# Performance work log

Measured on AMD Instinct MI355X. Metric: run time of the kernel, lower is better.

## Reference

```python
import jax, jax.numpy as jnp
import numpy as np

ALPHA = 0.2      # LeakyReLU negative slope
EPS = 1e-5       # LayerNorm eps
NEG = -9e15


def setup_inputs() -> dict:
    key = jax.random.key(0)
    ks = jax.random.split(key, 7)
    B, N, F_in, F_out = 8, 1024, 512, 512
    h1 = jax.random.normal(ks[0], (B, N, F_in), jnp.float32)
    h2 = jax.random.normal(ks[1], (B, N, F_in), jnp.float32)
    adj = jax.random.randint(ks[2], (B, N, N), 0, 2, jnp.int32)
    s = 1.414 * (6.0 / (F_in + F_out)) ** 0.5  # xavier_uniform gain=1.414
    W1 = jax.random.uniform(ks[3], (F_in, F_out), jnp.float32, -s, s)
    W2 = jax.random.uniform(ks[4], (F_in, F_out), jnp.float32, -s, s)
    W3 = jax.random.uniform(ks[5], (F_in, F_out), jnp.float32, -s, s)
    sa = 1.414 * (6.0 / (2 * F_out + 1)) ** 0.5
    a = jax.random.uniform(ks[6], (2 * F_out, 1), jnp.float32, -sa, sa)
    gamma = jnp.ones((F_out,), jnp.float32)
    beta = jnp.zeros((F_out,), jnp.float32)
    return {"h1": h1, "h2": h2, "adj": adj, "W1": W1, "W2": W2,
            "W3": W3, "a": a, "gamma": gamma, "beta": beta}


def reference(h1, h2, adj, W1, W2, W3, a, gamma, beta):
    F_out = W1.shape[1]
    Wh = h1 @ W1                      # [B,N,F]
    Wt = h2 @ W2                      # [B,N,F]
    a1 = a[:F_out, 0]                 # [F]
    a2 = a[F_out:, 0]                 # [F]
    # decomposed edge score: cat([Wh_i, Wt_j]) @ a == Wh_i@a1 + Wt_j@a2
    e = (Wh @ a1)[:, :, None] + (Wt @ a2)[:, None, :]   # [B,N,N]
    e = jnp.where(e > 0, e, ALPHA * e)                  # LeakyReLU
    e = jnp.where(adj > 0, e, NEG)
    attention = jax.nn.softmax(e, axis=2)               # [B,N,N]
    Wv = h2 @ W3                                        # [B,N,F]
    h_prime = attention @ Wv                            # [B,N,F]
    mu = jnp.mean(h_prime, axis=-1, keepdims=True)
    var = jnp.mean(jnp.square(h_prime - mu), axis=-1, keepdims=True)
    h_prime = (h_prime - mu) * jax.lax.rsqrt(var + EPS) * gamma + beta
    return jax.nn.gelu(h_prime, approximate=False)
```

## Files before the change

kernel.cpp:

```cpp
#include <hip/hip_runtime.h>
#include <math.h>

#define ALPHA 0.2f
#define NEGV  -9000000000000000.0f
#define EPSV  1e-5f

static constexpr int Bn = 8;
static constexpr int Nn = 1024;
static constexpr int Fn = 512;
static constexpr int M  = Bn * Nn;

typedef __attribute__((ext_vector_type(8))) short bf16x8;
typedef __attribute__((ext_vector_type(4))) float f32x4;

__device__ inline float wave_reduce_sum(float v) {
#pragma unroll
    for (int off = 32; off; off >>= 1) v += __shfl_xor(v, off);
    return v;
}
__device__ inline float wave_reduce_max(float v) {
#pragma unroll
    for (int off = 32; off; off >>= 1) v = fmaxf(v, __shfl_xor(v, off));
    return v;
}

__device__ inline unsigned short bf16_rne(float f) {
    union { float f; unsigned int u; } v; v.f = f;
    unsigned int r = v.u + 0x7FFFu + ((v.u >> 16) & 1u);
    return (unsigned short)(r >> 16);
}
__device__ inline float bf16_to_f(unsigned short h) {
    union { unsigned int u; float f; } v; v.u = (unsigned int)h << 16;
    return v.f;
}

__global__ __launch_bounds__(256) void k_pack(const int* __restrict__ adj,
                                              unsigned int* __restrict__ pk) {
    int idx = blockIdx.x * 256 + threadIdx.x;
    const int* p = adj + (size_t)idx * 32;
    unsigned int m = 0;
#pragma unroll
    for (int q = 0; q < 8; ++q) {
        int4 v = *(const int4*)&p[q * 4];
        m |= (unsigned)(v.x > 0) << (q * 4 + 0);
        m |= (unsigned)(v.y > 0) << (q * 4 + 1);
        m |= (unsigned)(v.z > 0) << (q * 4 + 2);
        m |= (unsigned)(v.w > 0) << (q * 4 + 3);
    }
    pk[idx] = m;
}

__global__ __launch_bounds__(64) void k_proj_w(const float* __restrict__ W1,
                                               const float* __restrict__ W2,
                                               const float* __restrict__ a,
                                               float* __restrict__ c) {
    int bid = blockIdx.x, which = bid >> 9, row = bid & 511;
    const float* W  = which ? W2 : W1;
    const float* av = a + which * Fn;
    const float* wr = W + (size_t)row * Fn;
    int lane = threadIdx.x;
    float s = 0.f;
#pragma unroll
    for (int p = 0; p < 2; ++p) {
        float4 wv = *(const float4*)&wr[lane * 4 + p * 256];
        float4 a4 = *(const float4*)&av[lane * 4 + p * 256];
        s += wv.x * a4.x + wv.y * a4.y + wv.z * a4.z + wv.w * a4.w;
    }
    s = wave_reduce_sum(s);
    if (lane == 0) c[which * Fn + row] = s;
}

__global__ __launch_bounds__(256) void k_proj_h(const float* __restrict__ h1,
                                                const float* __restrict__ h2,
                                                const float* __restrict__ c,
                                                float* __restrict__ Wha,
                                                float* __restrict__ Wta) {
    int which = blockIdx.y;
    const float* h  = which ? h2 : h1;
    const float* cv = c + which * Fn;
    float* outp = which ? Wta : Wha;
    int wave = threadIdx.x >> 6, lane = threadIdx.x & 63;
    int row  = blockIdx.x * 4 + wave;
    const float* hr = h + (size_t)row * Fn;
    float s = 0.f;
#pragma unroll
    for (int p = 0; p < 2; ++p) {
        float4 hv = *(const float4*)&hr[lane * 8 + p * 4];
        float4 c4 = *(const float4*)&cv[lane * 8 + p * 4];
        s += hv.x * c4.x + hv.y * c4.y + hv.z * c4.z + hv.w * c4.w;
    }
    s = wave_reduce_sum(s);
    if (lane == 0) outp[row] = s;
}

__global__ __launch_bounds__(256) void k_w3t(const float* __restrict__ W3,
                                             unsigned short* __restrict__ hi,
                                             unsigned short* __restrict__ lo) {
    __shared__ float tile[32][33];
    int kt = blockIdx.x * 32, ft = blockIdx.y * 32;
    int c = threadIdx.x & 31, r = threadIdx.x >> 5;
#pragma unroll
    for (int s = 0; s < 4; ++s)
        tile[r + s * 8][c] = W3[(size_t)(kt + r + s * 8) * Fn + ft + c];
    __syncthreads();
#pragma unroll
    for (int s = 0; s < 4; ++s) {
        float f = tile[c][r + s * 8];
        unsigned short h = bf16_rne(f);
        size_t o = (size_t)(ft + r + s * 8) * Fn + kt + c;
        hi[o] = h;
        lo[o] = bf16_rne(f - bf16_to_f(h));
    }
}

__global__ __launch_bounds__(256) void k_gemm2(const float* __restrict__ h2,
                                               const unsigned short* __restrict__ w3h,
                                               const unsigned short* __restrict__ w3l,
                                               unsigned short* __restrict__ wvh,
                                               unsigned short* __restrict__ wvl) {
    __shared__ float etile[64 * 132];
    int t = threadIdx.x, wave = t >> 6, lane = t & 63;
    int l15 = lane & 15, l16 = lane >> 4;
    int i0 = blockIdx.x * 128, f0 = blockIdx.y * 64;
    int wr = wave;

    f32x4 acc[2][4];
#pragma unroll
    for (int mi = 0; mi < 2; ++mi)
#pragma unroll
        for (int nj = 0; nj < 4; ++nj) acc[mi][nj] = (f32x4){0.f, 0.f, 0.f, 0.f};

    const float* a0base = h2 + (size_t)(i0 + wr * 32 + l15) * Fn + l16 * 8;
    const float* a1base = a0base + 16 * Fn;
    const unsigned short* bhb = w3h + (size_t)(f0 + l15) * Fn + l16 * 8;
    const unsigned short* blb = w3l + (size_t)(f0 + l15) * Fn + l16 * 8;

#pragma unroll 2
    for (int kt = 0; kt < Fn / 32; ++kt) {
        bf16x8 bh[4], bl[4];
#pragma unroll
        for (int nj = 0; nj < 4; ++nj) {
            bh[nj] = *(const bf16x8*)(bhb + (size_t)nj * 16 * Fn + kt * 32);
            bl[nj] = *(const bf16x8*)(blb + (size_t)nj * 16 * Fn + kt * 32);
        }
        float4 v0 = *(const float4*)(a0base + kt * 32);
        float4 v1 = *(const float4*)(a0base + kt * 32 + 4);
        float4 v2 = *(const float4*)(a1base + kt * 32);
        float4 v3 = *(const float4*)(a1base + kt * 32 + 4);
        bf16x8 a0, a1;
        {
            const float* f0p = (const float*)&v0;
            const float* f1p = (const float*)&v2;
#pragma unroll
            for (int q = 0; q < 4; ++q) {
                a0[q] = (short)bf16_rne(f0p[q]);
                a1[q] = (short)bf16_rne(f1p[q]);
            }
            const float* g0p = (const float*)&v1;
            const float* g1p = (const float*)&v3;
#pragma unroll
            for (int q = 0; q < 4; ++q) {
                a0[4 + q] = (short)bf16_rne(g0p[q]);
                a1[4 + q] = (short)bf16_rne(g1p[q]);
            }
        }
#pragma unroll
        for (int nj = 0; nj < 4; ++nj) {
            acc[0][nj] = __builtin_amdgcn_mfma_f32_16x16x32_bf16(a0, bh[nj], acc[0][nj], 0, 0, 0);
            acc[0][nj] = __builtin_amdgcn_mfma_f32_16x16x32_bf16(a0, bl[nj], acc[0][nj], 0, 0, 0);
            acc[1][nj] = __builtin_amdgcn_mfma_f32_16x16x32_bf16(a1, bh[nj], acc[1][nj], 0, 0, 0);
            acc[1][nj] = __builtin_amdgcn_mfma_f32_16x16x32_bf16(a1, bl[nj], acc[1][nj], 0, 0, 0);
        }
    }
#pragma unroll
    for (int mi = 0; mi < 2; ++mi)
#pragma unroll
        for (int nj = 0; nj < 4; ++nj) {
            int nloc = wr * 32 + mi * 16 + l16 * 4;
            int floc = nj * 16 + l15;
            *(float4*)&etile[floc * 132 + nloc] = *(float4*)&acc[mi][nj];
        }
    __syncthreads();
    {
        int floc = t >> 2, n0 = (t & 3) * 32;
        int b = i0 >> 10, nb = i0 & 1023;
        unsigned short* oh = wvh + ((size_t)b * Fn + f0 + floc) * Nn + nb + n0;
        unsigned short* ol = wvl + ((size_t)b * Fn + f0 + floc) * Nn + nb + n0;
        const float* src = &etile[floc * 132 + n0];
        bf16x8 rh[4], rl[4];
#pragma unroll
        for (int s = 0; s < 4; ++s) {
#pragma unroll
            for (int q = 0; q < 8; ++q) {
                float f = src[s * 8 + q];
                unsigned short h = bf16_rne(f);
                rh[s][q] = (short)h;
                rl[s][q] = (short)bf16_rne(f - bf16_to_f(h));
            }
        }
#pragma unroll
        for (int s = 0; s < 4; ++s) {
            *(bf16x8*)(oh + s * 8) = rh[s];
            *(bf16x8*)(ol + s * 8) = rl[s];
        }
    }
}

__global__ __launch_bounds__(256) void k_stats(const unsigned int* __restrict__ pk,
                                               const float* __restrict__ Wha,
                                               const float* __restrict__ Wta,
                                               float2* __restrict__ stat) {
    int bi = blockIdx.x;
    int b = bi >> 10;
    const float* wt = Wta + b * Nn;
    float whai = Wha[bi];
    int t = threadIdx.x;
    unsigned int word = pk[(size_t)bi * 32 + (t >> 3)];
    int sh = (t & 7) * 4;
    float4 wv = *(const float4*)&wt[t * 4];
    float e[4];
    {
        float x;
        x = whai + wv.x; x = fmaxf(x, ALPHA * x); e[0] = ((word >> (sh + 0)) & 1) ? x : NEGV;
        x = whai + wv.y; x = fmaxf(x, ALPHA * x); e[1] = ((word >> (sh + 1)) & 1) ? x : NEGV;
        x = whai + wv.z; x = fmaxf(x, ALPHA * x); e[2] = ((word >> (sh + 2)) & 1) ? x : NEGV;
        x = whai + wv.w; x = fmaxf(x, ALPHA * x); e[3] = ((word >> (sh + 3)) & 1) ? x : NEGV;
    }
    float m4 = fmaxf(fmaxf(e[0], e[1]), fmaxf(e[2], e[3]));
    __shared__ float redm[4], reds[4];
    int wave = t >> 6, lane = t & 63;
    float m = wave_reduce_max(m4);
    if (lane == 0) redm[wave] = m;
    __syncthreads();
    m = fmaxf(fmaxf(redm[0], redm[1]), fmaxf(redm[2], redm[3]));
    float s4 = __expf(e[0] - m) + __expf(e[1] - m) + __expf(e[2] - m) + __expf(e[3] - m);
    float s = wave_reduce_sum(s4);
    if (lane == 0) reds[wave] = s;
    __syncthreads();
    if (t == 0) {
        s = reds[0] + reds[1] + reds[2] + reds[3];
        stat[bi] = make_float2(m, 1.0f / s);
    }
}

__global__ __launch_bounds__(256) void k_attn2(const unsigned int* __restrict__ pk,
                                               const float* __restrict__ Wha,
                                               const float* __restrict__ Wta,
                                               const float2* __restrict__ stat,
                                               const unsigned short* __restrict__ wvh,
                                               const unsigned short* __restrict__ wvl,
                                               float* __restrict__ outp) {
    __shared__ unsigned int pkt[32 * 128];
    __shared__ float wta_s[Nn];
    __shared__ float wha_s[128], m_s[128], rs_s[128];
    int t = threadIdx.x, wave = t >> 6, lane = t & 63;
    int l15 = lane & 15, l16 = lane >> 4;
    int f0 = blockIdx.x * 64, i0 = blockIdx.y * 128, b = blockIdx.z;

    {
        int r = t >> 1, half = t & 1;
        const unsigned int* src = pk + ((size_t)(b * Nn + i0 + r)) * 32 + half * 16;
        uint4 w0 = *(const uint4*)src, w1 = *(const uint4*)(src + 4);
        uint4 w2 = *(const uint4*)(src + 8), w3 = *(const uint4*)(src + 12);
        const unsigned int* ww = (const unsigned int*)&w0;
        unsigned int wv_[16] = {w0.x, w0.y, w0.z, w0.w, w1.x, w1.y, w1.z, w1.w,
                                w2.x, w2.y, w2.z, w2.w, w3.x, w3.y, w3.z, w3.w};
        (void)ww;
#pragma unroll
        for (int w = 0; w < 16; ++w) pkt[(half * 16 + w) * 128 + r] = wv_[w];
        *(float4*)&wta_s[t * 4] = *(const float4*)&Wta[b * Nn + t * 4];
        if (t < 128) {
            wha_s[t] = Wha[b * Nn + i0 + t];
            float2 st = stat[b * Nn + i0 + t];
            m_s[t] = st.x; rs_s[t] = st.y;
        }
    }
    __syncthreads();

    int wr = wave;
    float whaA = wha_s[wr * 32 + l15],      mA = m_s[wr * 32 + l15];
    float whaB = wha_s[wr * 32 + 16 + l15], mB = m_s[wr * 32 + 16 + l15];
    const unsigned short* bhb = wvh + ((size_t)b * Fn + f0 + l15) * Nn + l16 * 8;
    const unsigned short* blb = wvl + ((size_t)b * Fn + f0 + l15) * Nn + l16 * 8;

    f32x4 acc[2][4];
#pragma unroll
    for (int mi = 0; mi < 2; ++mi)
#pragma unroll
        for (int nj = 0; nj < 4; ++nj) acc[mi][nj] = (f32x4){0.f, 0.f, 0.f, 0.f};

#pragma unroll 2
    for (int kt = 0; kt < Nn / 32; ++kt) {
        bf16x8 bh[4], bl[4];
#pragma unroll
        for (int nj = 0; nj < 4; ++nj) {
            bh[nj] = *(const bf16x8*)(bhb + (size_t)nj * 16 * Nn + kt * 32);
            bl[nj] = *(const bf16x8*)(blb + (size_t)nj * 16 * Nn + kt * 32);
        }
        unsigned int shA = pkt[kt * 128 + wr * 32 + l15] >> (l16 * 8);
        unsigned int shB = pkt[kt * 128 + wr * 32 + 16 + l15] >> (l16 * 8);
        float4 wq0 = *(const float4*)&wta_s[kt * 32 + l16 * 8];
        float4 wq1 = *(const float4*)&wta_s[kt * 32 + l16 * 8 + 4];
        float wq[8] = {wq0.x, wq0.y, wq0.z, wq0.w, wq1.x, wq1.y, wq1.z, wq1.w};
        bf16x8 a0, a1;
#pragma unroll
        for (int q = 0; q < 8; ++q) {
            float xA = whaA + wq[q];
            xA = fmaxf(xA, ALPHA * xA);
            float pA = __expf(xA - mA);
            pA = ((shA >> q) & 1) ? pA : 0.0f;
            a0[q] = (short)bf16_rne(pA);
            float xB = whaB + wq[q];
            xB = fmaxf(xB, ALPHA * xB);
            float pB = __expf(xB - mB);
            pB = ((shB >> q) & 1) ? pB : 0.0f;
            a1[q] = (short)bf16_rne(pB);
        }
#pragma unroll
        for (int nj = 0; nj < 4; ++nj) {
            acc[0][nj] = __builtin_amdgcn_mfma_f32_16x16x32_bf16(a0, bh[nj], acc[0][nj], 0, 0, 0);
            acc[0][nj] = __builtin_amdgcn_mfma_f32_16x16x32_bf16(a0, bl[nj], acc[0][nj], 0, 0, 0);
            acc[1][nj] = __builtin_amdgcn_mfma_f32_16x16x32_bf16(a1, bh[nj], acc[1][nj], 0, 0, 0);
            acc[1][nj] = __builtin_amdgcn_mfma_f32_16x16x32_bf16(a1, bl[nj], acc[1][nj], 0, 0, 0);
        }
    }
#pragma unroll
    for (int mi = 0; mi < 2; ++mi)
#pragma unroll
        for (int nj = 0; nj < 4; ++nj) {
#pragma unroll
            for (int r = 0; r < 4; ++r) {
                int rloc = wr * 32 + mi * 16 + l16 * 4 + r;
                float rs = rs_s[rloc];
                outp[((size_t)b * Nn + i0 + rloc) * Fn + f0 + nj * 16 + l15] =
                    rs * acc[mi][nj][r];
            }
        }
}

__global__ __launch_bounds__(128) void k_ln_gelu(float* __restrict__ x,
                                                 const float* __restrict__ gamma,
                                                 const float* __restrict__ beta) {
    int row = blockIdx.x;
    float* xr = x + (size_t)row * Fn;
    int t = threadIdx.x;
    float4 v = *(float4*)&xr[t * 4];
    float s = v.x + v.y + v.z + v.w;
    float q = v.x * v.x + v.y * v.y + v.z * v.z + v.w * v.w;
    s = wave_reduce_sum(s);
    q = wave_reduce_sum(q);
    __shared__ float rs[2], rq[2];
    int wave = t >> 6, lane = t & 63;
    if (lane == 0) { rs[wave] = s; rq[wave] = q; }
    __syncthreads();
    s = rs[0] + rs[1];
    q = rq[0] + rq[1];
    float mu   = s * (1.0f / Fn);
    float var  = q * (1.0f / Fn) - mu * mu;
    float rstd = rsqrtf(var + EPSV);
    float4 g  = *(const float4*)&gamma[t * 4];
    float4 be = *(const float4*)&beta[t * 4];
    auto gel = [](float xx) { return 0.5f * xx * (1.0f + erff(xx * 0.70710678118f)); };
    float y0 = (v.x - mu) * rstd * g.x + be.x;
    float y1 = (v.y - mu) * rstd * g.y + be.y;
    float y2 = (v.z - mu) * rstd * g.z + be.z;
    float y3 = (v.w - mu) * rstd * g.w + be.w;
    float4 o = {gel(y0), gel(y1), gel(y2), gel(y3)};
    *(float4*)&xr[t * 4] = o;
}

extern "C" void kernel_launch(void* const* d_in, const int* in_sizes, int n_in,
                              void* d_out, int out_size, void* d_ws, size_t ws_size,
                              hipStream_t stream) {
    const float* h1    = (const float*)d_in[0];
    const float* h2    = (const float*)d_in[1];
    const int*   adj   = (const int*)d_in[2];
    const float* W1    = (const float*)d_in[3];
    const float* W2    = (const float*)d_in[4];
    const float* W3    = (const float*)d_in[5];
    const float* a     = (const float*)d_in[6];
    const float* gamma = (const float*)d_in[7];
    const float* beta  = (const float*)d_in[8];
    float* outp = (float*)d_out;

    unsigned short* wvh  = (unsigned short*)d_ws;
    unsigned short* wvl  = wvh + (size_t)M * Fn;
    unsigned short* w3h  = wvl + (size_t)M * Fn;
    unsigned short* w3l  = w3h + (size_t)Fn * Fn;
    unsigned int*   pack = (unsigned int*)(w3l + (size_t)Fn * Fn);
    float2*         stat = (float2*)(pack + (size_t)M * 32);
    float*          c    = (float*)(stat + M);
    float*          Wha  = c + 1024;
    float*          Wta  = Wha + M;

    hipLaunchKernelGGL(k_pack, dim3(M * 32 / 256), dim3(256), 0, stream, adj, pack);
    hipLaunchKernelGGL(k_proj_w, dim3(1024), dim3(64), 0, stream, W1, W2, a, c);
    hipLaunchKernelGGL(k_proj_h, dim3(M / 4, 2), dim3(256), 0, stream, h1, h2, c, Wha, Wta);
    hipLaunchKernelGGL(k_w3t, dim3(16, 16), dim3(256), 0, stream, W3, w3h, w3l);
    hipLaunchKernelGGL(k_gemm2, dim3(M / 128, Fn / 64), dim3(256), 0, stream,
                       h2, w3h, w3l, wvh, wvl);
    hipLaunchKernelGGL(k_stats, dim3(M), dim3(256), 0, stream, pack, Wha, Wta, stat);
    hipLaunchKernelGGL(k_attn2, dim3(Fn / 64, Nn / 128, Bn), dim3(256), 0, stream,
                       pack, Wha, Wta, stat, wvh, wvl, outp);
    hipLaunchKernelGGL(k_ln_gelu, dim3(M), dim3(128), 0, stream, outp, gamma, beta);
}
```

Measured before the change: 245.5 us.

## Fuse adjacency packing with softmax stats and halve GEMM row tiles

Merges the adjacency bit-packing kernel and the row softmax-statistics kernel into one pass over adj, so the packed mask is not written and then reread by a separate launch. The value GEMM and the attention GEMM now use 64-row tiles with one 16-row MFMA strip per wave and launch_bounds hinting four blocks per CU. This doubles the grid and lowers register pressure to raise occupancy, at the cost of less reuse of each B-fragment load across rows. The hand-written bf16 rounding is also replaced with the HIP intrinsic.

```diff
diff --git a/kernel.cpp b/kernel.cpp
--- a/kernel.cpp
+++ b/kernel.cpp
@@ -1,4 +1,5 @@
 #include <hip/hip_runtime.h>
+#include <hip/hip_bf16.h>
 #include <math.h>
 
 #define ALPHA 0.2f
@@ -24,30 +25,13 @@
     return v;
 }
 
-__device__ inline unsigned short bf16_rne(float f) {
-    union { float f; unsigned int u; } v; v.f = f;
-    unsigned int r = v.u + 0x7FFFu + ((v.u >> 16) & 1u);
-    return (unsigned short)(r >> 16);
-}
-__device__ inline float bf16_to_f(unsigned short h) {
-    union { unsigned int u; float f; } v; v.u = (unsigned int)h << 16;
+__device__ inline short f2bf(float f) {
+    __hip_bfloat16 h = __float2bfloat16(f);
+    return *reinterpret_cast<short*>(&h);
+}
+__device__ inline float bf2f(short s) {
+    union { unsigned int u; float f; } v; v.u = (unsigned int)(unsigned short)s << 16;
     return v.f;
-}
-
-__global__ __launch_bounds__(256) void k_pack(const int* __restrict__ adj,
-                                              unsigned int* __restrict__ pk) {
-    int idx = blockIdx.x * 256 + threadIdx.x;
-    const int* p = adj + (size_t)idx * 32;
-    unsigned int m = 0;
-#pragma unroll
-    for (int q = 0; q < 8; ++q) {
-        int4 v = *(const int4*)&p[q * 4];
-        m |= (unsigned)(v.x > 0) << (q * 4 + 0);
-        m |= (unsigned)(v.y > 0) << (q * 4 + 1);
-        m |= (unsigned)(v.z > 0) << (q * 4 + 2);
-        m |= (unsigned)(v.w > 0) << (q * 4 + 3);
-    }
-    pk[idx] = m;
 }
 
 __global__ __launch_bounds__(64) void k_proj_w(const float* __restrict__ W1,
@@ -93,6 +77,54 @@
     if (lane == 0) outp[row] = s;
 }
 
+__global__ __launch_bounds__(256) void k_packstats(const int* __restrict__ adj,
+                                                   const float* __restrict__ Wha,
+                                                   const float* __restrict__ Wta,
+                                                   unsigned int* __restrict__ pk,
+                                                   float2* __restrict__ stat) {
+    int bi = blockIdx.x;
+    int b = bi >> 10;
+    const int*   arow = adj + (size_t)bi * Nn;
+    const float* wt   = Wta + b * Nn;
+    float whai = Wha[bi];
+    int t = threadIdx.x;
+    int4   av = *(const int4*)&arow[t * 4];
+    float4 wv = *(const float4*)&wt[t * 4];
+    unsigned int nib = (unsigned)(av.x > 0) | ((unsigned)(av.y > 0) << 1) |
+                       ((unsigned)(av.z > 0) << 2) | ((unsigned)(av.w > 0) << 3);
+    float e[4];
+    {
+        float x;
+        x = whai + wv.x; x = fmaxf(x, ALPHA * x); e[0] = (nib & 1) ? x : NEGV;
+        x = whai + wv.y; x = fmaxf(x, ALPHA * x); e[1] = (nib & 2) ? x : NEGV;
+        x = whai + wv.z; x = fmaxf(x, ALPHA * x); e[2] = (nib & 4) ? x : NEGV;
+        x = whai + wv.w; x = fmaxf(x, ALPHA * x); e[3] = (nib & 8) ? x : NEGV;
+    }
+    __shared__ unsigned char nibs[256];
+    __shared__ float redm[4], reds[4];
+    nibs[t] = (unsigned char)nib;
+    int wave = t >> 6, lane = t & 63;
+    float m4 = fmaxf(fmaxf(e[0], e[1]), fmaxf(e[2], e[3]));
+    float m = wave_reduce_max(m4);
+    if (lane == 0) redm[wave] = m;
+    __syncthreads();
+    m = fmaxf(fmaxf(redm[0], redm[1]), fmaxf(redm[2], redm[3]));
+    float s4 = __expf(e[0] - m) + __expf(e[1] - m) + __expf(e[2] - m) + __expf(e[3] - m);
+    float s = wave_reduce_sum(s4);
+    if (lane == 0) reds[wave] = s;
+    __syncthreads();
+    if (t < 32) {
+        unsigned int w = 0;
+#pragma unroll
+        for (int u = 0; u < 8; ++u) w |= ((unsigned int)nibs[t * 8 + u]) << (4 * u);
+        pk[(size_t)bi * 32 + t] = w;
+    }
+    if (t == 0) {
+        s = reds[0] + reds[1] + reds[2] + reds[3];
+        stat[bi] = make_float2(m, 1.0f / s);
+    }
+}
+
 __global__ __launch_bounds__(256) void k_w3t(const float* __restrict__ W3,
                                              unsigned short* __restrict__ hi,
                                              unsigned short* __restrict__ lo) {
@@ -106,32 +138,28 @@
 #pragma unroll
     for (int s = 0; s < 4; ++s) {
         float f = tile[c][r + s * 8];
-        unsigned short h = bf16_rne(f);
+        short h = f2bf(f);
         size_t o = (size_t)(ft + r + s * 8) * Fn + kt + c;
-        hi[o] = h;
-        lo[o] = bf16_rne(f - bf16_to_f(h));
-    }
-}
-
-__global__ __launch_bounds__(256) void k_gemm2(const float* __restrict__ h2,
-                                               const unsigned short* __restrict__ w3h,
-                                               const unsigned short* __restrict__ w3l,
-                                               unsigned short* __restrict__ wvh,
-                                               unsigned short* __restrict__ wvl) {
-    __shared__ float etile[64 * 132];
+        hi[o] = (unsigned short)h;
+        lo[o] = (unsigned short)f2bf(f - bf2f(h));
+    }
+}
+
+__global__ __launch_bounds__(256, 4) void k_gemm3(const float* __restrict__ h2,
+                                                  const unsigned short* __restrict__ w3h,
+                                                  const unsigned short* __restrict__ w3l,
+                                                  unsigned short* __restrict__ wvh,
+                                                  unsigned short* __restrict__ wvl) {
+    __shared__ float etile[64 * 68];
     int t = threadIdx.x, wave = t >> 6, lane = t & 63;
     int l15 = lane & 15, l16 = lane >> 4;
-    int i0 = blockIdx.x * 128, f0 = blockIdx.y * 64;
-    int wr = wave;
-
-    f32x4 acc[2][4];
-#pragma unroll
-    for (int mi = 0; mi < 2; ++mi)
-#pragma unroll
-        for (int nj = 0; nj < 4; ++nj) acc[mi][nj] = (f32x4){0.f, 0.f, 0.f, 0.f};
-
-    const float* a0base = h2 + (size_t)(i0 + wr * 32 + l15) * Fn + l16 * 8;
-    const float* a1base = a0base + 16 * Fn;
+    int i0 = blockIdx.x * 64, f0 = blockIdx.y * 64;
+
+    f32x4 acc[4];
+#pragma unroll
+    for (int nj = 0; nj < 4; ++nj) acc[nj] = (f32x4){0.f, 0.f, 0.f, 0.f};
+
+    const float* abase = h2 + (size_t)(i0 + wave * 16 + l15) * Fn + l16 * 8;
     const unsigned short* bhb = w3h + (size_t)(f0 + l15) * Fn + l16 * 8;
     const unsigned short* blb = w3l + (size_t)(f0 + l15) * Fn + l16 * 8;
 
@@ -143,133 +171,68 @@
             bh[nj] = *(const bf16x8*)(bhb + (size_t)nj * 16 * Fn + kt * 32);
             bl[nj] = *(const bf16x8*)(blb + (size_t)nj * 16 * Fn + kt * 32);
         }
-        float4 v0 = *(const float4*)(a0base + kt * 32);
-        float4 v1 = *(const float4*)(a0base + kt * 32 + 4);
-        float4 v2 = *(const float4*)(a1base + kt * 32);
-        float4 v3 = *(const float4*)(a1base + kt * 32 + 4);
-        bf16x8 a0, a1;
-        {
-            const float* f0p = (const float*)&v0;
-            const float* f1p = (const float*)&v2;
-#pragma unroll
-            for (int q = 0; q < 4; ++q) {
-                a0[q] = (short)bf16_rne(f0p[q]);
-                a1[q] = (short)bf16_rne(f1p[q]);
-            }
-            const float* g0p = (const float*)&v1;
-            const float* g1p = (const float*)&v3;
-#pragma unroll
-            for (int q = 0; q < 4; ++q) {
-                a0[4 + q] = (short)bf16_rne(g0p[q]);
-                a1[4 + q] = (short)bf16_rne(g1p[q]);
-            }
-        }
+        float4 v0 = *(const float4*)(abase + kt * 32);
+        float4 v1 = *(const float4*)(abase + kt * 32 + 4);
+        bf16x8 a0;
+        a0[0] = f2bf(v0.x); a0[1] = f2bf(v0.y); a0[2] = f2bf(v0.z); a0[3] = f2bf(v0.w);
+        a0[4] = f2bf(v1.x); a0[5] = f2bf(v1.y); a0[6] = f2bf(v1.z); a0[7] = f2bf(v1.w);
 #pragma unroll
         for (int nj = 0; nj < 4; ++nj) {
-            acc[0][nj] = __builtin_amdgcn_mfma_f32_16x16x32_bf16(a0, bh[nj], acc[0][nj], 0, 0, 0);
-            acc[0][nj] = __builtin_amdgcn_mfma_f32_16x16x32_bf16(a0, bl[nj], acc[0][nj], 0, 0, 0);
-            acc[1][nj] = __builtin_amdgcn_mfma_f32_16x16x32_bf16(a1, bh[nj], acc[1][nj], 0, 0, 0);
-            acc[1][nj] = __builtin_amdgcn_mfma_f32_16x16x32_bf16(a1, bl[nj], acc[1][nj], 0, 0, 0);
-        }
-    }
-#pragma unroll
-    for (int mi = 0; mi < 2; ++mi)
-#pragma unroll
-        for (int nj = 0; nj < 4; ++nj) {
-            int nloc = wr * 32 + mi * 16 + l16 * 4;
-            int floc = nj * 16 + l15;
-            *(float4*)&etile[floc * 132 + nloc] = *(float4*)&acc[mi][nj];
-        }
+            acc[nj] = __builtin_amdgcn_mfma_f32_16x16x32_bf16(a0, bh[nj], acc[nj], 0, 0, 0);
+            acc[nj] = __builtin_amdgcn_mfma_f32_16x16x32_bf16(a0, bl[nj], acc[nj], 0, 0, 0);
+        }
+    }
+#pragma unroll
+    for (int nj = 0; nj < 4; ++nj) {
+        int floc = nj * 16 + l15;
+        int nloc = wave * 16 + l16 * 4;
+        *(f32x4*)&etile[floc * 68 + nloc] = acc[nj];
+    }
     __syncthreads();
     {
-        int floc = t >> 2, n0 = (t & 3) * 32;
-        int b = i0 >> 10, nb = i0 & 1023;
-        unsigned short* oh = wvh + ((size_t)b * Fn + f0 + floc) * Nn + nb + n0;
-        unsigned short* ol = wvl + ((size_t)b * Fn + f0 + floc) * Nn + nb + n0;
-        const float* src = &etile[floc * 132 + n0];
-        bf16x8 rh[4], rl[4];
-#pragma unroll
-        for (int s = 0; s < 4; ++s) {
-#pragma unroll
-            for (int q = 0; q < 8; ++q) {
-                float f = src[s * 8 + q];
-                unsigned short h = bf16_rne(f);
-                rh[s][q] = (short)h;
-                rl[s][q] = (short)bf16_rne(f - bf16_to_f(h));
-            }
-        }
-#pragma unroll
-        for (int s = 0; s < 4; ++s) {
-            *(bf16x8*)(oh + s * 8) = rh[s];
-            *(bf16x8*)(ol + s * 8) = rl[s];
-        }
-    }
-}
-
-__global__ __launch_bounds__(256) void k_stats(const unsigned int* __restrict__ pk,
-                                               const float* __restrict__ Wha,
-                                               const float* __restrict__ Wta,
-                                               float2* __restrict__ stat) {
-    int bi = blockIdx.x;
-    int b = bi >> 10;
-    const float* wt = Wta + b * Nn;
-    float whai = Wha[bi];
-    int t = threadIdx.x;
-    unsigned int word = pk[(size_t)bi * 32 + (t >> 3)];
-    int sh = (t & 7) * 4;
-    float4 wv = *(const float4*)&wt[t * 4];
-    float e[4];
-    {
-        float x;
-        x = whai + wv.x; x = fmaxf(x, ALPHA * x); e[0] = ((word >> (sh + 0)) & 1) ? x : NEGV;
-        x = whai + wv.y; x = fmaxf(x, ALPHA * x); e[1] = ((word >> (sh + 1)) & 1) ? x : NEGV;
-        x = whai + wv.z; x = fmaxf(x, ALPHA * x); e[2] = ((word >> (sh + 2)) & 1) ? x : NEGV;
-        x = whai + wv.w; x = fmaxf(x, ALPHA * x); e[3] = ((word >> (sh + 3)) & 1) ? x : NEGV;
-    }
-    float m4 = fmaxf(fmaxf(e[0], e[1]), fmaxf(e[2], e[3]));
-    __shared__ float redm[4], reds[4];
-    int wave = t >> 6, lane = t & 63;
-    float m = wave_reduce_max(m4);
-    if (lane == 0) redm[wave] = m;
-    __syncthreads();
-    m = fmaxf(fmaxf(redm[0], redm[1]), fmaxf(redm[2], redm[3]));
-    float s4 = __expf(e[0] - m) + __expf(e[1] - m) + __expf(e[2] - m) + __expf(e[3] - m);
-    float s = wave_reduce_sum(s4);
-    if (lane == 0) reds[wave] = s;
-    __syncthreads();
-    if (t == 0) {
-        s = reds[0] + reds[1] + reds[2] + reds[3];
-        stat[bi] = make_float2(m, 1.0f / s);
-    }
-}
-
-__global__ __launch_bounds__(256) void k_attn2(const unsigned int* __restrict__ pk,
-                                               const float* __restrict__ Wha,
-                                               const float* __restrict__ Wta,
-                                               const float2* __restrict__ stat,
-                                               const unsigned short* __restrict__ wvh,
-                                               const unsigned short* __restrict__ wvl,
-                                               float* __restrict__ outp) {
-    __shared__ unsigned int pkt[32 * 128];
+        int floc = t >> 2, ic = (t & 3) * 16;
+        int b = i0 >> 10, nb = (i0 & 1023) + ic;
+        const float* src = &etile[floc * 68 + ic];
+        unsigned short* oh = wvh + ((size_t)b * Fn + f0 + floc) * Nn + nb;
+        unsigned short* ol = wvl + ((size_t)b * Fn + f0 + floc) * Nn + nb;
+        bf16x8 rh0, rh1, rl0, rl1;
+#pragma unroll
+        for (int q = 0; q < 8; ++q) {
+            float f0v = src[q], f1v = src[8 + q];
+            short h0 = f2bf(f0v), h1 = f2bf(f1v);
+            rh0[q] = h0; rh1[q] = h1;
+            rl0[q] = f2bf(f0v - bf2f(h0));
+            rl1[q] = f2bf(f1v - bf2f(h1));
+        }
+        *(bf16x8*)oh = rh0; *(bf16x8*)(oh + 8) = rh1;
+        *(bf16x8*)ol = rl0; *(bf16x8*)(ol + 8) = rl1;
+    }
+}
+
+__global__ __launch_bounds__(256, 4) void k_attn3(const unsigned int* __restrict__ pk,
+                                                  const float* __restrict__ Wha,
+                                                  const float* __restrict__ Wta,
+                                                  const float2* __restrict__ stat,
+                                                  const unsigned short* __restrict__ wvh,
+                                                  const unsigned short* __restrict__ wvl,
+                                                  float* __restrict__ outp) {
+    __shared__ unsigned int pkt[32 * 64];
     __shared__ float wta_s[Nn];
-    __shared__ float wha_s[128], m_s[128], rs_s[128];
+    __shared__ float wha_s[64], m_s[64], rs_s[64];
     int t = threadIdx.x, wave = t >> 6, lane = t & 63;
     int l15 = lane & 15, l16 = lane >> 4;
-    int f0 = blockIdx.x * 64, i0 = blockIdx.y * 128, b = blockIdx.z;
+    int f0 = blockIdx.x * 64, i0 = blockIdx.y * 64, b = blockIdx.z;
 
     {
-        int r = t >> 1, half = t & 1;
-        const unsigned int* src = pk + ((size_t)(b * Nn + i0 + r)) * 32 + half * 16;
-        uint4 w0 = *(const uint4*)src, w1 = *(const uint4*)(src + 4);
-        uint4 w2 = *(const uint4*)(src + 8), w3 = *(const uint4*)(src + 12);
-        const unsigned int* ww = (const unsigned int*)&w0;
-        unsigned int wv_[16] = {w0.x, w0.y, w0.z, w0.w, w1.x, w1.y, w1.z, w1.w,
-                                w2.x, w2.y, w2.z, w2.w, w3.x, w3.y, w3.z, w3.w};
-        (void)ww;
-#pragma unroll
-        for (int w = 0; w < 16; ++w) pkt[(half * 16 + w) * 128 + r] = wv_[w];
+        int r = t & 63, wq = t >> 6;
+        const unsigned int* src = pk + (size_t)(b * Nn + i0 + r) * 32 + wq * 8;
+        uint4 u0 = *(const uint4*)src, u1 = *(const uint4*)(src + 4);
+        pkt[(wq * 8 + 0) * 64 + r] = u0.x; pkt[(wq * 8 + 1) * 64 + r] = u0.y;
+        pkt[(wq * 8 + 2) * 64 + r] = u0.z; pkt[(wq * 8 + 3) * 64 + r] = u0.w;
+        pkt[(wq * 8 + 4) * 64 + r] = u1.x; pkt[(wq * 8 + 5) * 64 + r] = u1.y;
+        pkt[(wq * 8 + 6) * 64 + r] = u1.z; pkt[(wq * 8 + 7) * 64 + r] = u1.w;
         *(float4*)&wta_s[t * 4] = *(const float4*)&Wta[b * Nn + t * 4];
-        if (t < 128) {
+        if (t < 64) {
             wha_s[t] = Wha[b * Nn + i0 + t];
             float2 st = stat[b * Nn + i0 + t];
             m_s[t] = st.x; rs_s[t] = st.y;
@@ -277,17 +240,14 @@
     }
     __syncthreads();
 
-    int wr = wave;
-    float whaA = wha_s[wr * 32 + l15],      mA = m_s[wr * 32 + l15];
-    float whaB = wha_s[wr * 32 + 16 + l15], mB = m_s[wr * 32 + 16 + l15];
+    float whaA = wha_s[wave * 16 + l15];
+    float mA   = m_s[wave * 16 + l15];
     const unsigned short* bhb = wvh + ((size_t)b * Fn + f0 + l15) * Nn + l16 * 8;
     const unsigned short* blb = wvl + ((size_t)b * Fn + f0 + l15) * Nn + l16 * 8;
 
-    f32x4 acc[2][4];
-#pragma unroll
-    for (int mi = 0; mi < 2; ++mi)
-#pragma unroll
-        for (int nj = 0; nj < 4; ++nj) acc[mi][nj] = (f32x4){0.f, 0.f, 0.f, 0.f};
+    f32x4 acc[4];
+#pragma unroll
+    for (int nj = 0; nj < 4; ++nj) acc[nj] = (f32x4){0.f, 0.f, 0.f, 0.f};
 
 #pragma unroll 2
     for (int kt = 0; kt < Nn / 32; ++kt) {
@@ -297,45 +257,34 @@
             bh[nj] = *(const bf16x8*)(bhb + (size_t)nj * 16 * Nn + kt * 32);
             bl[nj] = *(const bf16x8*)(blb + (size_t)nj * 16 * Nn + kt * 32);
         }
-        unsigned int shA = pkt[kt * 128 + wr * 32 + l15] >> (l16 * 8);
-        unsigned int shB = pkt[kt * 128 + wr * 32 + 16 + l15] >> (l16 * 8);
+        unsigned int sh = pkt[kt * 64 + wave * 16 + l15] >> (l16 * 8);
         float4 wq0 = *(const float4*)&wta_s[kt * 32 + l16 * 8];
         float4 wq1 = *(const float4*)&wta_s[kt * 32 + l16 * 8 + 4];
         float wq[8] = {wq0.x, wq0.y, wq0.z, wq0.w, wq1.x, wq1.y, wq1.z, wq1.w};
-        bf16x8 a0, a1;
+        bf16x8 a0;
 #pragma unroll
         for (int q = 0; q < 8; ++q) {
-            float xA = whaA + wq[q];
-            xA = fmaxf(xA, ALPHA * xA);
-            float pA = __expf(xA - mA);
-            pA = ((shA >> q) & 1) ? pA : 0.0f;
-            a0[q] = (short)bf16_rne(pA);
-            float xB = whaB + wq[q];
-            xB = fmaxf(xB, ALPHA * xB);
-            float pB = __expf(xB - mB);
-            pB = ((shB >> q) & 1) ? pB : 0.0f;
-            a1[q] = (short)bf16_rne(pB);
+            float x = whaA + wq[q];
+            x = fmaxf(x, ALPHA * x);
+            float p = __expf(x - mA);
+            p = ((sh >> q) & 1) ? p : 0.0f;
+            a0[q] = f2bf(p);
         }
 #pragma unroll
         for (int nj = 0; nj < 4; ++nj) {
-            acc[0][nj] = __builtin_amdgcn_mfma_f32_16x16x32_bf16(a0, bh[nj], acc[0][nj], 0, 0, 0);
-            acc[0][nj] = __builtin_amdgcn_mfma_f32_16x16x32_bf16(a0, bl[nj], acc[0][nj], 0, 0, 0);
-            acc[1][nj] = __builtin_amdgcn_mfma_f32_16x16x32_bf16(a1, bh[nj], acc[1][nj], 0, 0, 0);
-            acc[1][nj] = __builtin_amdgcn_mfma_f32_16x16x32_bf16(a1, bl[nj], acc[1][nj], 0, 0, 0);
-        }
-    }
-#pragma unroll
-    for (int mi = 0; mi < 2; ++mi)
-#pragma unroll
-        for (int nj = 0; nj < 4; ++nj) {
-#pragma unroll
-            for (int r = 0; r < 4; ++r) {
-                int rloc = wr * 32 + mi * 16 + l16 * 4 + r;
-                float rs = rs_s[rloc];
-                outp[((size_t)b * Nn + i0 + rloc) * Fn + f0 + nj * 16 + l15] =
-                    rs * acc[mi][nj][r];
-            }
-        }
+            acc[nj] = __builtin_amdgcn_mfma_f32_16x16x32_bf16(a0, bh[nj], acc[nj], 0, 0, 0);
+            acc[nj] = __builtin_amdgcn_mfma_f32_16x16x32_bf16(a0, bl[nj], acc[nj], 0, 0, 0);
+        }
+    }
+#pragma unroll
+    for (int nj = 0; nj < 4; ++nj) {
+#pragma unroll
+        for (int r = 0; r < 4; ++r) {
+            int rloc = wave * 16 + l16 * 4 + r;
+            outp[((size_t)b * Nn + i0 + rloc) * Fn + f0 + nj * 16 + l15] =
+                rs_s[rloc] * acc[nj][r];
+        }
+    }
 }
 
 __global__ __launch_bounds__(128) void k_ln_gelu(float* __restrict__ x,
@@ -393,14 +342,13 @@
     float*          Wha  = c + 1024;
     float*          Wta  = Wha + M;
 
-    hipLaunchKernelGGL(k_pack, dim3(M * 32 / 256), dim3(256), 0, stream, adj, pack);
     hipLaunchKernelGGL(k_proj_w, dim3(1024), dim3(64), 0, stream, W1, W2, a, c);
     hipLaunchKernelGGL(k_proj_h, dim3(M / 4, 2), dim3(256), 0, stream, h1, h2, c, Wha, Wta);
+    hipLaunchKernelGGL(k_packstats, dim3(M), dim3(256), 0, stream, adj, Wha, Wta, pack, stat);
     hipLaunchKernelGGL(k_w3t, dim3(16, 16), dim3(256), 0, stream, W3, w3h, w3l);
-    hipLaunchKernelGGL(k_gemm2, dim3(M / 128, Fn / 64), dim3(256), 0, stream,
+    hipLaunchKernelGGL(k_gemm3, dim3(M / 64, Fn / 64), dim3(256), 0, stream,
                        h2, w3h, w3l, wvh, wvl);
-    hipLaunchKernelGGL(k_stats, dim3(M), dim3(256), 0, stream, pack, Wha, Wta, stat);
-    hipLaunchKernelGGL(k_attn2, dim3(Fn / 64, Nn / 128, Bn), dim3(256), 0, stream,
+    hipLaunchKernelGGL(k_attn3, dim3(Fn / 64, Nn / 64, Bn), dim3(256), 0, stream,
                        pack, Wha, Wta, stat, wvh, wvl, outp);
     hipLaunchKernelGGL(k_ln_gelu, dim3(M), dim3(128), 0, stream, outp, gamma, beta);
 }
```

Measured after the change: 318.4 us. 29.7% more time.
